# Optimization experiments

Measured on AMD Instinct MI355X. Metric: run time of the kernel, lower is better.

Reference implementation:

```python
import jax, jax.numpy as jnp
import numpy as np

N, M, K = 500000, 8, 16


def setup_inputs() -> dict:
    key = jax.random.key(0)
    kp, kq, ka, kx = jax.random.split(key, 4)
    p = jax.random.normal(kp, (N, M), dtype=jnp.float32)
    q = jax.random.normal(kq, (N, M), dtype=jnp.float32)
    # scale transitions to be contractive so the length-N recurrence is stable
    a = 0.2 * jax.random.normal(ka, (N, M, M), dtype=jnp.float32)
    x = jax.random.normal(kx, (N, K), dtype=jnp.float32)
    return {"p": p, "q": q, "a": a, "x": x}


def reference(p, q, a, x):
    # StrictLowerTriQSM.matmul: y_i = p_i @ f_i, with recurrence
    # f_{i+1} = a_i @ f_i + outer(q_i, x_i), f_0 = 0.  f has shape (M, K).
    def impl(f, data):
        qi, ai, xi = data
        return ai @ f + jnp.outer(qi, xi), f

    init = jnp.zeros((M, x.shape[1]), dtype=x.dtype)
    _, f = jax.lax.scan(impl, init, (q, a, x))  # f: (N, M, K)
    return jnp.einsum("nm,nmk->nk", p, f)
```

## Files before the change

### kernel.cpp

```cpp
#include <hip/hip_runtime.h>


#define NTOT 500000
#define CHUNK 64
#define NCHUNK 8192
#define G 4
#define NGPC 16
#define GRPSZ 64
#define NGRP 128
#define CLAMPI 499996

#define OFF_AGGA  0u
#define OFF_AGGB  524288u
#define OFF_GAGA  1572864u
#define OFF_GAGB  1581056u

#define AS1(p) ((const __attribute__((address_space(1))) void*)(p))
#define AS3(p) ((__attribute__((address_space(3))) void*)(p))
#define GLOAD_LDS16(gp, lp) __builtin_amdgcn_global_load_lds(AS1(gp), AS3(lp), 16, 0, 0)
#define GLOAD_LDS4(gp, lp)  __builtin_amdgcn_global_load_lds(AS1(gp), AS3(lp), 4, 0, 0)
#define WAIT_VM(n) asm volatile("s_waitcnt vmcnt(" #n ")" ::: "memory")

static __device__ __forceinline__ int iminc(int a, int b) { return a < b ? a : b; }

__global__ __launch_bounds__(256, 4) void k1_aggregate(
    const float* __restrict__ q, const float* __restrict__ a,
    const float* __restrict__ x, float* __restrict__ ws)
{
  __shared__ float sm[4 * 2 * 704];
  const int wv   = (int)(threadIdx.x >> 6);
  const int wave = blockIdx.x * 4 + wv;
  const int lane = (int)(threadIdx.x & 63);
  const int sub  = lane >> 5;
  const int ll   = lane & 31;
  const int c    = wave * 2 + sub;
  const bool isB = ll < 16;
  const bool isA = (ll >= 16) && (ll < 24);
  const int bcol = ll & 15;
  const int acol = (ll - 16) & 7;

  float* wbuf = sm + wv * 1408;
  const int c0 = wave * 2, c1 = c0 + 1;

  float v[8];
#pragma unroll
  for (int m = 0; m < 8; ++m) v[m] = 0.f;
  if (isA) v[acol] = 1.f;

  int cnt = NTOT - c * CHUNK;
  cnt = cnt < 0 ? 0 : (cnt > CHUNK ? CHUNK : cnt);

  auto stage = [&](int g, float* lb) {
    const int b0 = iminc(c0 * CHUNK + g * G, CLAMPI);
    const int b1 = iminc(c1 * CHUNK + g * G, CLAMPI);
    GLOAD_LDS16(a + (size_t)b0 * 64u + lane * 4, lb);
    GLOAD_LDS16(a + (size_t)b1 * 64u + lane * 4, lb + 256);
    GLOAD_LDS4(q + (size_t)(lane < 32 ? b0 : b1) * 8u + ll, lb + 512);
    GLOAD_LDS4(x + (size_t)b0 * 16u + lane, lb + 576);
    GLOAD_LDS4(x + (size_t)b1 * 16u + lane, lb + 640);
  };

  stage(0, wbuf);
#pragma unroll 1
  for (int g = 0; g < NGPC; ++g) {
    float* lb = wbuf + (g & 1) * 704;
    if (g + 1 < NGPC) {
      stage(g + 1, wbuf + ((g + 1) & 1) * 704);
      WAIT_VM(5);
    } else {
      WAIT_VM(0);
    }
#pragma unroll 1
    for (int e = 0; e < G; ++e) {
      const int eg = g * G + e;
      if (eg < cnt) {
        const float* ae = lb + sub * 256 + e * 64;
        const float xk  = lb[576 + sub * 64 + e * 16 + bcol];
        const float* qe = lb + 512 + sub * 32 + e * 8;
        float qv[8];
        *(float4*)&qv[0] = *(const float4*)(qe);
        *(float4*)&qv[4] = *(const float4*)(qe + 4);
        float nv[8];
#pragma unroll
        for (int m = 0; m < 8; ++m) {
          float4 r0 = *(const float4*)(ae + m * 8);
          float4 r1 = *(const float4*)(ae + m * 8 + 4);
          float s = isB ? (qv[m] * xk) : 0.f;
          s += r0.x * v[0] + r0.y * v[1] + r0.z * v[2] + r0.w * v[3]
             + r1.x * v[4] + r1.y * v[5] + r1.z * v[6] + r1.w * v[7];
          nv[m] = s;
        }
#pragma unroll
        for (int m = 0; m < 8; ++m) v[m] = nv[m];
      }
    }
  }

  if (isB) {
    float* dst = ws + OFF_AGGB + (size_t)c * 128u + (size_t)bcol * 8u;
#pragma unroll
    for (int m = 0; m < 8; ++m) dst[m] = v[m];
  } else if (isA) {
    float* dst = ws + OFF_AGGA + (size_t)c * 64u + (size_t)acol * 8u;
#pragma unroll
    for (int m = 0; m < 8; ++m) dst[m] = v[m];
  }
}

__global__ __launch_bounds__(64) void k2a_groupscan(float* __restrict__ ws)
{
  __shared__ float sA[GRPSZ * 64];
  const int g    = blockIdx.x;
  const int lane = (int)(threadIdx.x & 63);
  const bool isB = lane < 16;
  const bool isA = (lane >= 16) && (lane < 24);
  const int bcol = lane & 15;
  const int acol = (lane - 16) & 7;

#pragma unroll 1
  for (int t = 0; t < 16; ++t)
    GLOAD_LDS16(ws + OFF_AGGA + (size_t)g * (GRPSZ * 64u) + t * 256 + lane * 4,
                sA + t * 256);

  float v[8];
#pragma unroll
  for (int m = 0; m < 8; ++m) v[m] = 0.f;
  if (isA) v[acol] = 1.f;

  float4 nb0, nb1;
  {
    const float* s = ws + OFF_AGGB + (size_t)(g * GRPSZ) * 128u + (size_t)bcol * 8u;
    nb0 = *(const float4*)s; nb1 = *(const float4*)(s + 4);
  }
  WAIT_VM(0);

#pragma unroll 1
  for (int j = 0; j < GRPSZ; ++j) {
    const int c = g * GRPSZ + j;
    float bB[8] = {nb0.x, nb0.y, nb0.z, nb0.w, nb1.x, nb1.y, nb1.z, nb1.w};
    if (j + 1 < GRPSZ) {
      const float* s = ws + OFF_AGGB + (size_t)(c + 1) * 128u + (size_t)bcol * 8u;
      nb0 = *(const float4*)s; nb1 = *(const float4*)(s + 4);
    }
    if (isB) {
      float* dst = ws + OFF_AGGB + (size_t)c * 128u + (size_t)bcol * 8u;
#pragma unroll
      for (int m = 0; m < 8; ++m) dst[m] = v[m];
    } else if (isA) {
      float* dst = ws + OFF_AGGA + (size_t)c * 64u + (size_t)acol * 8u;
#pragma unroll
      for (int m = 0; m < 8; ++m) dst[m] = v[m];
    }
    const float* Aj = sA + j * 64;
    float nv[8];
#pragma unroll
    for (int m = 0; m < 8; ++m) nv[m] = 0.f;
#pragma unroll
    for (int t = 0; t < 8; ++t) {
      float4 col0 = *(const float4*)(Aj + t * 8);
      float4 col1 = *(const float4*)(Aj + t * 8 + 4);
      nv[0] += col0.x * v[t]; nv[1] += col0.y * v[t];
      nv[2] += col0.z * v[t]; nv[3] += col0.w * v[t];
      nv[4] += col1.x * v[t]; nv[5] += col1.y * v[t];
      nv[6] += col1.z * v[t]; nv[7] += col1.w * v[t];
    }
    if (isB) {
#pragma unroll
      for (int m = 0; m < 8; ++m) nv[m] += bB[m];
    }
#pragma unroll
    for (int m = 0; m < 8; ++m) v[m] = nv[m];
  }

  if (isB) {
    float* dst = ws + OFF_GAGB + (size_t)g * 128u + (size_t)bcol * 8u;
#pragma unroll
    for (int m = 0; m < 8; ++m) dst[m] = v[m];
  } else if (isA) {
    float* dst = ws + OFF_GAGA + (size_t)g * 64u + (size_t)acol * 8u;
#pragma unroll
    for (int m = 0; m < 8; ++m) dst[m] = v[m];
  }
}

__global__ __launch_bounds__(64) void k2b_topscan(float* __restrict__ ws)
{
  __shared__ float sA[NGRP * 64];
  const int lane = (int)(threadIdx.x & 63);
  const bool isB = lane < 16;
  const bool isA = (lane >= 16) && (lane < 24);
  const int bcol = lane & 15;
  const int acol = (lane - 16) & 7;

#pragma unroll 1
  for (int t = 0; t < 32; ++t)
    GLOAD_LDS16(ws + OFF_GAGA + t * 256 + lane * 4, sA + t * 256);

  float v[8];
#pragma unroll
  for (int m = 0; m < 8; ++m) v[m] = 0.f;
  if (isA) v[acol] = 1.f;

  float4 nb0, nb1;
  {
    const float* s = ws + OFF_GAGB + (size_t)bcol * 8u;
    nb0 = *(const float4*)s; nb1 = *(const float4*)(s + 4);
  }
  WAIT_VM(0);

#pragma unroll 1
  for (int j = 0; j < NGRP; ++j) {
    float bB[8] = {nb0.x, nb0.y, nb0.z, nb0.w, nb1.x, nb1.y, nb1.z, nb1.w};
    if (j + 1 < NGRP) {
      const float* s = ws + OFF_GAGB + (size_t)(j + 1) * 128u + (size_t)bcol * 8u;
      nb0 = *(const float4*)s; nb1 = *(const float4*)(s + 4);
    }
    if (isB) {
      float* dst = ws + OFF_GAGB + (size_t)j * 128u + (size_t)bcol * 8u;
#pragma unroll
      for (int m = 0; m < 8; ++m) dst[m] = v[m];
    }
    const float* Aj = sA + j * 64;
    float nv[8];
#pragma unroll
    for (int m = 0; m < 8; ++m) nv[m] = 0.f;
#pragma unroll
    for (int t = 0; t < 8; ++t) {
      float4 col0 = *(const float4*)(Aj + t * 8);
      float4 col1 = *(const float4*)(Aj + t * 8 + 4);
      nv[0] += col0.x * v[t]; nv[1] += col0.y * v[t];
      nv[2] += col0.z * v[t]; nv[3] += col0.w * v[t];
      nv[4] += col1.x * v[t]; nv[5] += col1.y * v[t];
      nv[6] += col1.z * v[t]; nv[7] += col1.w * v[t];
    }
    if (isB) {
#pragma unroll
      for (int m = 0; m < 8; ++m) nv[m] += bB[m];
    }
#pragma unroll
    for (int m = 0; m < 8; ++m) v[m] = nv[m];
  }
}

#define K3_BQ 1040
#define K3_BP 1172
#define K3_BX 1304
#define K3_BUF 1624
__global__ __launch_bounds__(256, 3) void k3_output(
    const float* __restrict__ p, const float* __restrict__ q,
    const float* __restrict__ a, const float* __restrict__ x,
    const float* __restrict__ ws, float* __restrict__ out)
{
  __shared__ float sm3[4 * 2 * K3_BUF];
  const int wv   = (int)(threadIdx.x >> 6);
  const int wave = blockIdx.x * 4 + wv;
  const int lane = (int)(threadIdx.x & 63);
  const int sub  = lane >> 4;
  const int k    = lane & 15;
  const int c    = wave * 4 + sub;
  const int grp  = c >> 6;

  float* wbuf = sm3 + wv * (2 * K3_BUF);
  const int cb = wave * 4;

  auto stage = [&](int g, float* lb) {
    int b[4];
#pragma unroll
    for (int cc = 0; cc < 4; ++cc) b[cc] = iminc((cb + cc) * CHUNK + g * G, CLAMPI);
    GLOAD_LDS16(a + (size_t)b[0] * 64u + lane * 4, lb);
    GLOAD_LDS16(a + (size_t)b[1] * 64u + lane * 4, lb + 260);
    GLOAD_LDS16(a + (size_t)b[2] * 64u + lane * 4, lb + 520);
    GLOAD_LDS16(a + (size_t)b[3] * 64u + lane * 4, lb + 780);
    GLOAD_LDS4(q + (size_t)(lane < 32 ? b[0] : b[1]) * 8u + (lane & 31), lb + K3_BQ);
    GLOAD_LDS4(q + (size_t)(lane < 32 ? b[2] : b[3]) * 8u + (lane & 31), lb + K3_BQ + 68);
    GLOAD_LDS4(p + (size_t)(lane < 32 ? b[0] : b[1]) * 8u + (lane & 31), lb + K3_BP);
    GLOAD_LDS4(p + (size_t)(lane < 32 ? b[2] : b[3]) * 8u + (lane & 31), lb + K3_BP + 68);
    GLOAD_LDS4(x + (size_t)b[0] * 16u + lane, lb + K3_BX);
    GLOAD_LDS4(x + (size_t)b[1] * 16u + lane, lb + K3_BX + 80);
    GLOAD_LDS4(x + (size_t)b[2] * 16u + lane, lb + K3_BX + 160);
    GLOAD_LDS4(x + (size_t)b[3] * 16u + lane, lb + K3_BX + 240);
  };

  stage(0, wbuf);

  const float* __restrict__ pA = ws + OFF_AGGA + (size_t)c * 64u;
  float af[64];
#pragma unroll
  for (int t = 0; t < 64; ++t) af[t] = pA[t];
  const float* __restrict__ gBp = ws + OFF_GAGB + (size_t)grp * 128u + (size_t)k * 8u;
  const float* __restrict__ lBp = ws + OFF_AGGB + (size_t)c * 128u + (size_t)k * 8u;
  float gcol[8];
#pragma unroll
  for (int t = 0; t < 8; ++t) gcol[t] = gBp[t];
  float f[8];
#pragma unroll
  for (int m = 0; m < 8; ++m) {
    float s = lBp[m];
#pragma unroll
    for (int t = 0; t < 8; ++t) s += af[t * 8 + m] * gcol[t];
    f[m] = s;
  }

  int cnt = NTOT - c * CHUNK;
  cnt = cnt < 0 ? 0 : (cnt > CHUNK ? CHUNK : cnt);

#pragma unroll 1
  for (int g = 0; g < NGPC; ++g) {
    float* lb = wbuf + (g & 1) * K3_BUF;
    if (g + 1 < NGPC) {
      stage(g + 1, wbuf + ((g + 1) & 1) * K3_BUF);
      WAIT_VM(12);
    } else {
      WAIT_VM(0);
    }
#pragma unroll 1
    for (int e = 0; e < G; ++e) {
      const int eg = g * G + e;
      if (eg < cnt) {
        const int i = c * CHUNK + eg;
        const float* ae = lb + sub * 260 + e * 64;
        const float* qe = lb + K3_BQ + (sub >> 1) * 68 + (sub & 1) * 32 + e * 8;
        const float* pe = lb + K3_BP + (sub >> 1) * 68 + (sub & 1) * 32 + e * 8;
        const float xk  = lb[K3_BX + sub * 80 + e * 16 + k];
        float qv[8], pv[8];
        *(float4*)&qv[0] = *(const float4*)(qe);
        *(float4*)&qv[4] = *(const float4*)(qe + 4);
        *(float4*)&pv[0] = *(const float4*)(pe);
        *(float4*)&pv[4] = *(const float4*)(pe + 4);

        float y = 0.f;
#pragma unroll
        for (int m = 0; m < 8; ++m) y += pv[m] * f[m];
        out[(size_t)i * 16u + k] = y;

        float nf[8];
#pragma unroll
        for (int m = 0; m < 8; ++m) {
          float4 r0 = *(const float4*)(ae + m * 8);
          float4 r1 = *(const float4*)(ae + m * 8 + 4);
          float s = qv[m] * xk;
          s += r0.x * f[0] + r0.y * f[1] + r0.z * f[2] + r0.w * f[3]
             + r1.x * f[4] + r1.y * f[5] + r1.z * f[6] + r1.w * f[7];
          nf[m] = s;
        }
#pragma unroll
        for (int m = 0; m < 8; ++m) f[m] = nf[m];
      }
    }
  }
}

extern "C" void kernel_launch(void* const* d_in, const int* in_sizes, int n_in,
                              void* d_out, int out_size, void* d_ws, size_t ws_size,
                              hipStream_t stream)
{
  const float* p = (const float*)d_in[0];
  const float* q = (const float*)d_in[1];
  const float* a = (const float*)d_in[2];
  const float* x = (const float*)d_in[3];
  float* out = (float*)d_out;
  float* ws  = (float*)d_ws;

  hipLaunchKernelGGL(k1_aggregate, dim3(NCHUNK / 2 / 4), dim3(256), 0, stream, q, a, x, ws);
  hipLaunchKernelGGL(k2a_groupscan, dim3(NGRP), dim3(64), 0, stream, ws);
  hipLaunchKernelGGL(k2b_topscan, dim3(1), dim3(64), 0, stream, ws);
  hipLaunchKernelGGL(k3_output, dim3(NCHUNK / 4 / 4), dim3(256), 0, stream, p, q, a, x, ws, out);
}
```

Measured before the change: 196.6 us.

## Triple-buffer LDS prefetch and halve chunks per wave in output kernel

Both the aggregate and output kernels move from double to triple buffering of the global-to-LDS staged loads, keeping two groups of loads in flight to hide more memory latency. The output kernel now handles 2 chunks per wave instead of 4, so half the lanes are idle, and it launches twice as many blocks. It also reads the chunk aggregate matrix directly instead of holding 64 floats in registers, which lowers register pressure and allows 4 waves per SIMD. The trade-off is more LDS per block, half-utilised waves in the output kernel, and more waves doing the same sequential work.

```diff
diff --git a/kernel.cpp b/kernel.cpp
--- a/kernel.cpp
+++ b/kernel.cpp
@@ -27,7 +27,7 @@
     const float* __restrict__ q, const float* __restrict__ a,
     const float* __restrict__ x, float* __restrict__ ws)
 {
-  __shared__ float sm[4 * 2 * 704];
+  __shared__ float sm[4 * 3 * 704];
   const int wv   = (int)(threadIdx.x >> 6);
   const int wave = blockIdx.x * 4 + wv;
   const int lane = (int)(threadIdx.x & 63);
@@ -39,8 +39,10 @@
   const int bcol = ll & 15;
   const int acol = (ll - 16) & 7;
 
-  float* wbuf = sm + wv * 1408;
   const int c0 = wave * 2, c1 = c0 + 1;
+  float* b0 = sm + wv * 2112;
+  float* b1 = b0 + 704;
+  float* b2 = b0 + 1408;
 
   float v[8];
 #pragma unroll
@@ -51,21 +53,24 @@
   cnt = cnt < 0 ? 0 : (cnt > CHUNK ? CHUNK : cnt);
 
   auto stage = [&](int g, float* lb) {
-    const int b0 = iminc(c0 * CHUNK + g * G, CLAMPI);
-    const int b1 = iminc(c1 * CHUNK + g * G, CLAMPI);
-    GLOAD_LDS16(a + (size_t)b0 * 64u + lane * 4, lb);
-    GLOAD_LDS16(a + (size_t)b1 * 64u + lane * 4, lb + 256);
-    GLOAD_LDS4(q + (size_t)(lane < 32 ? b0 : b1) * 8u + ll, lb + 512);
-    GLOAD_LDS4(x + (size_t)b0 * 16u + lane, lb + 576);
-    GLOAD_LDS4(x + (size_t)b1 * 16u + lane, lb + 640);
+    const int e0 = iminc(c0 * CHUNK + g * G, CLAMPI);
+    const int e1 = iminc(c1 * CHUNK + g * G, CLAMPI);
+    GLOAD_LDS16(a + (size_t)e0 * 64u + lane * 4, lb);
+    GLOAD_LDS16(a + (size_t)e1 * 64u + lane * 4, lb + 256);
+    GLOAD_LDS4(q + (size_t)(lane < 32 ? e0 : e1) * 8u + ll, lb + 512);
+    GLOAD_LDS4(x + (size_t)e0 * 16u + lane, lb + 576);
+    GLOAD_LDS4(x + (size_t)e1 * 16u + lane, lb + 640);
   };
 
-  stage(0, wbuf);
+  stage(0, b0);
+  stage(1, b1);
 #pragma unroll 1
   for (int g = 0; g < NGPC; ++g) {
-    float* lb = wbuf + (g & 1) * 704;
-    if (g + 1 < NGPC) {
-      stage(g + 1, wbuf + ((g + 1) & 1) * 704);
+    float* lb = b0;
+    if (g + 2 < NGPC) {
+      stage(g + 2, b2);
+      WAIT_VM(10);
+    } else if (g + 1 < NGPC) {
       WAIT_VM(5);
     } else {
       WAIT_VM(0);
@@ -76,6 +81,7 @@
       if (eg < cnt) {
         const float* ae = lb + sub * 256 + e * 64;
         const float xk  = lb[576 + sub * 64 + e * 16 + bcol];
+        const float xke = isB ? xk : 0.f;
         const float* qe = lb + 512 + sub * 32 + e * 8;
         float qv[8];
         *(float4*)&qv[0] = *(const float4*)(qe);
@@ -85,7 +91,7 @@
         for (int m = 0; m < 8; ++m) {
           float4 r0 = *(const float4*)(ae + m * 8);
           float4 r1 = *(const float4*)(ae + m * 8 + 4);
-          float s = isB ? (qv[m] * xk) : 0.f;
+          float s = qv[m] * xke;
           s += r0.x * v[0] + r0.y * v[1] + r0.z * v[2] + r0.w * v[3]
              + r1.x * v[4] + r1.y * v[5] + r1.z * v[6] + r1.w * v[7];
           nv[m] = s;
@@ -94,6 +100,7 @@
         for (int m = 0; m < 8; ++m) v[m] = nv[m];
       }
     }
+    float* t = b0; b0 = b1; b1 = b2; b2 = t;
   }
 
   if (isB) {
@@ -242,51 +249,45 @@
   }
 }
 
-#define K3_BQ 1040
-#define K3_BP 1172
-#define K3_BX 1304
-#define K3_BUF 1624
-__global__ __launch_bounds__(256, 3) void k3_output(
+#define K3_BQ 520
+#define K3_BP 584
+#define K3_BX 648
+#define K3_BUF 784
+__global__ __launch_bounds__(256, 4) void k3_output(
     const float* __restrict__ p, const float* __restrict__ q,
     const float* __restrict__ a, const float* __restrict__ x,
     const float* __restrict__ ws, float* __restrict__ out)
 {
-  __shared__ float sm3[4 * 2 * K3_BUF];
+  __shared__ float sm3[4 * 3 * K3_BUF];
   const int wv   = (int)(threadIdx.x >> 6);
   const int wave = blockIdx.x * 4 + wv;
   const int lane = (int)(threadIdx.x & 63);
-  const int sub  = lane >> 4;
+  const int sub  = (lane >> 4) & 1;
   const int k    = lane & 15;
-  const int c    = wave * 4 + sub;
+  const bool active = lane < 32;
+  const int c    = wave * 2 + sub;
   const int grp  = c >> 6;
 
-  float* wbuf = sm3 + wv * (2 * K3_BUF);
-  const int cb = wave * 4;
+  const int c0 = wave * 2, c1 = c0 + 1;
+  float* b0 = sm3 + wv * (3 * K3_BUF);
+  float* b1 = b0 + K3_BUF;
+  float* b2 = b0 + 2 * K3_BUF;
 
   auto stage = [&](int g, float* lb) {
-    int b[4];
-#pragma unroll
-    for (int cc = 0; cc < 4; ++cc) b[cc] = iminc((cb + cc) * CHUNK + g * G, CLAMPI);
-    GLOAD_LDS16(a + (size_t)b[0] * 64u + lane * 4, lb);
-    GLOAD_LDS16(a + (size_t)b[1] * 64u + lane * 4, lb + 260);
-    GLOAD_LDS16(a + (size_t)b[2] * 64u + lane * 4, lb + 520);
-    GLOAD_LDS16(a + (size_t)b[3] * 64u + lane * 4, lb + 780);
-    GLOAD_LDS4(q + (size_t)(lane < 32 ? b[0] : b[1]) * 8u + (lane & 31), lb + K3_BQ);
-    GLOAD_LDS4(q + (size_t)(lane < 32 ? b[2] : b[3]) * 8u + (lane & 31), lb + K3_BQ + 68);
-    GLOAD_LDS4(p + (size_t)(lane < 32 ? b[0] : b[1]) * 8u + (lane & 31), lb + K3_BP);
-    GLOAD_LDS4(p + (size_t)(lane < 32 ? b[2] : b[3]) * 8u + (lane & 31), lb + K3_BP + 68);
-    GLOAD_LDS4(x + (size_t)b[0] * 16u + lane, lb + K3_BX);
-    GLOAD_LDS4(x + (size_t)b[1] * 16u + lane, lb + K3_BX + 80);
-    GLOAD_LDS4(x + (size_t)b[2] * 16u + lane, lb + K3_BX + 160);
-    GLOAD_LDS4(x + (size_t)b[3] * 16u + lane, lb + K3_BX + 240);
+    const int e0 = iminc(c0 * CHUNK + g * G, CLAMPI);
+    const int e1 = iminc(c1 * CHUNK + g * G, CLAMPI);
+    GLOAD_LDS16(a + (size_t)e0 * 64u + lane * 4, lb);
+    GLOAD_LDS16(a + (size_t)e1 * 64u + lane * 4, lb + 260);
+    GLOAD_LDS4(q + (size_t)(lane < 32 ? e0 : e1) * 8u + (lane & 31), lb + K3_BQ);
+    GLOAD_LDS4(p + (size_t)(lane < 32 ? e0 : e1) * 8u + (lane & 31), lb + K3_BP);
+    GLOAD_LDS4(x + (size_t)e0 * 16u + lane, lb + K3_BX);
+    GLOAD_LDS4(x + (size_t)e1 * 16u + lane, lb + K3_BX + 64);
   };
 
-  stage(0, wbuf);
-
-  const float* __restrict__ pA = ws + OFF_AGGA + (size_t)c * 64u;
-  float af[64];
-#pragma unroll
-  for (int t = 0; t < 64; ++t) af[t] = pA[t];
+  stage(0, b0);
+  stage(1, b1);
+
+  const float* __restrict__ pA  = ws + OFF_AGGA + (size_t)c * 64u;
   const float* __restrict__ gBp = ws + OFF_GAGB + (size_t)grp * 128u + (size_t)k * 8u;
   const float* __restrict__ lBp = ws + OFF_AGGB + (size_t)c * 128u + (size_t)k * 8u;
   float gcol[8];
@@ -294,11 +295,16 @@
   for (int t = 0; t < 8; ++t) gcol[t] = gBp[t];
   float f[8];
 #pragma unroll
-  for (int m = 0; m < 8; ++m) {
-    float s = lBp[m];
-#pragma unroll
-    for (int t = 0; t < 8; ++t) s += af[t * 8 + m] * gcol[t];
-    f[m] = s;
+  for (int m = 0; m < 8; ++m) f[m] = lBp[m];
+#pragma unroll
+  for (int t = 0; t < 8; ++t) {
+    float4 col0 = *(const float4*)(pA + t * 8);
+    float4 col1 = *(const float4*)(pA + t * 8 + 4);
+    const float gt = gcol[t];
+    f[0] += col0.x * gt; f[1] += col0.y * gt;
+    f[2] += col0.z * gt; f[3] += col0.w * gt;
+    f[4] += col1.x * gt; f[5] += col1.y * gt;
+    f[6] += col1.z * gt; f[7] += col1.w * gt;
   }
 
   int cnt = NTOT - c * CHUNK;
@@ -306,10 +312,12 @@
 
 #pragma unroll 1
   for (int g = 0; g < NGPC; ++g) {
-    float* lb = wbuf + (g & 1) * K3_BUF;
-    if (g + 1 < NGPC) {
-      stage(g + 1, wbuf + ((g + 1) & 1) * K3_BUF);
+    float* lb = b0;
+    if (g + 2 < NGPC) {
+      stage(g + 2, b2);
       WAIT_VM(12);
+    } else if (g + 1 < NGPC) {
+      WAIT_VM(6);
     } else {
       WAIT_VM(0);
     }
@@ -319,9 +327,9 @@
       if (eg < cnt) {
         const int i = c * CHUNK + eg;
         const float* ae = lb + sub * 260 + e * 64;
-        const float* qe = lb + K3_BQ + (sub >> 1) * 68 + (sub & 1) * 32 + e * 8;
-        const float* pe = lb + K3_BP + (sub >> 1) * 68 + (sub & 1) * 32 + e * 8;
-        const float xk  = lb[K3_BX + sub * 80 + e * 16 + k];
+        const float* qe = lb + K3_BQ + sub * 32 + e * 8;
+        const float* pe = lb + K3_BP + sub * 32 + e * 8;
+        const float xk  = lb[K3_BX + sub * 64 + e * 16 + k];
         float qv[8], pv[8];
         *(float4*)&qv[0] = *(const float4*)(qe);
         *(float4*)&qv[4] = *(const float4*)(qe + 4);
@@ -331,7 +339,7 @@
         float y = 0.f;
 #pragma unroll
         for (int m = 0; m < 8; ++m) y += pv[m] * f[m];
-        out[(size_t)i * 16u + k] = y;
+        if (active) out[(size_t)i * 16u + k] = y;
 
         float nf[8];
 #pragma unroll
@@ -347,6 +355,7 @@
         for (int m = 0; m < 8; ++m) f[m] = nf[m];
       }
     }
+    float* t = b0; b0 = b1; b1 = b2; b2 = t;
   }
 }
 
@@ -364,5 +373,5 @@
   hipLaunchKernelGGL(k1_aggregate, dim3(NCHUNK / 2 / 4), dim3(256), 0, stream, q, a, x, ws);
   hipLaunchKernelGGL(k2a_groupscan, dim3(NGRP), dim3(64), 0, stream, ws);
   hipLaunchKernelGGL(k2b_topscan, dim3(1), dim3(64), 0, stream, ws);
-  hipLaunchKernelGGL(k3_output, dim3(NCHUNK / 4 / 4), dim3(256), 0, stream, p, q, a, x, ws, out);
-}
+  hipLaunchKernelGGL(k3_output, dim3(NCHUNK / 2 / 4), dim3(256), 0, stream, p, q, a, x, ws, out);
+}
```

Measured after the change: 215.5 us. 1.1x slower.

## Triple-buffer LDS staging and pack four chunks per wave in aggregate kernel

Applied to the files above, without the earlier changes.

Both streaming kernels move from double- to triple-buffered global-to-LDS staging, with two stages in flight, to hide more memory latency. The aggregate kernel now handles four chunks per wave: each lane carries both a B column and an A column in registers, so all 64 lanes do useful work and the grid is halved. The output kernel reads the A aggregate with float4 loads instead of holding 64 registers. In exchange, LDS per block grows, the launch-bounds occupancy hint drops to 2, and per-lane work in k1 doubles.

```diff
diff --git a/kernel.cpp b/kernel.cpp
--- a/kernel.cpp
+++ b/kernel.cpp
@@ -23,87 +23,107 @@
 
 static __device__ __forceinline__ int iminc(int a, int b) { return a < b ? a : b; }
 
-__global__ __launch_bounds__(256, 4) void k1_aggregate(
+#define K1_BQ 1040
+#define K1_BX 1176
+#define K1_BUF 1480
+__global__ __launch_bounds__(256, 2) void k1_aggregate(
     const float* __restrict__ q, const float* __restrict__ a,
     const float* __restrict__ x, float* __restrict__ ws)
 {
-  __shared__ float sm[4 * 2 * 704];
+  __shared__ float sm[4 * 3 * K1_BUF];
   const int wv   = (int)(threadIdx.x >> 6);
   const int wave = blockIdx.x * 4 + wv;
   const int lane = (int)(threadIdx.x & 63);
-  const int sub  = lane >> 5;
-  const int ll   = lane & 31;
-  const int c    = wave * 2 + sub;
-  const bool isB = ll < 16;
-  const bool isA = (ll >= 16) && (ll < 24);
-  const int bcol = ll & 15;
-  const int acol = (ll - 16) & 7;
-
-  float* wbuf = sm + wv * 1408;
-  const int c0 = wave * 2, c1 = c0 + 1;
-
-  float v[8];
-#pragma unroll
-  for (int m = 0; m < 8; ++m) v[m] = 0.f;
-  if (isA) v[acol] = 1.f;
+  const int g    = lane >> 4;
+  const int ll   = lane & 15;
+  const int c    = wave * 4 + g;
+  const bool hasA = ll >= 8;
+  const int acol = ll & 7;
+
+  const int cb = wave * 4;
+  float* b0 = sm + wv * (3 * K1_BUF);
+  float* b1 = b0 + K1_BUF;
+  float* b2 = b0 + 2 * K1_BUF;
+
+  float vB[8], vA[8];
+#pragma unroll
+  for (int m = 0; m < 8; ++m) { vB[m] = 0.f; vA[m] = 0.f; }
+  if (hasA) vA[acol] = 1.f;
 
   int cnt = NTOT - c * CHUNK;
   cnt = cnt < 0 ? 0 : (cnt > CHUNK ? CHUNK : cnt);
 
-  auto stage = [&](int g, float* lb) {
-    const int b0 = iminc(c0 * CHUNK + g * G, CLAMPI);
-    const int b1 = iminc(c1 * CHUNK + g * G, CLAMPI);
-    GLOAD_LDS16(a + (size_t)b0 * 64u + lane * 4, lb);
-    GLOAD_LDS16(a + (size_t)b1 * 64u + lane * 4, lb + 256);
-    GLOAD_LDS4(q + (size_t)(lane < 32 ? b0 : b1) * 8u + ll, lb + 512);
-    GLOAD_LDS4(x + (size_t)b0 * 16u + lane, lb + 576);
-    GLOAD_LDS4(x + (size_t)b1 * 16u + lane, lb + 640);
+  auto stage = [&](int gg, float* lb) {
+    int b[4];
+#pragma unroll
+    for (int cc = 0; cc < 4; ++cc) b[cc] = iminc((cb + cc) * CHUNK + gg * G, CLAMPI);
+    GLOAD_LDS16(a + (size_t)b[0] * 64u + lane * 4, lb);
+    GLOAD_LDS16(a + (size_t)b[1] * 64u + lane * 4, lb + 260);
+    GLOAD_LDS16(a + (size_t)b[2] * 64u + lane * 4, lb + 520);
+    GLOAD_LDS16(a + (size_t)b[3] * 64u + lane * 4, lb + 780);
+    GLOAD_LDS4(q + (size_t)(lane < 32 ? b[0] : b[1]) * 8u + (lane & 31), lb + K1_BQ);
+    GLOAD_LDS4(q + (size_t)(lane < 32 ? b[2] : b[3]) * 8u + (lane & 31), lb + K1_BQ + 68);
+    GLOAD_LDS4(x + (size_t)b[0] * 16u + lane, lb + K1_BX);
+    GLOAD_LDS4(x + (size_t)b[1] * 16u + lane, lb + K1_BX + 80);
+    GLOAD_LDS4(x + (size_t)b[2] * 16u + lane, lb + K1_BX + 160);
+    GLOAD_LDS4(x + (size_t)b[3] * 16u + lane, lb + K1_BX + 240);
   };
 
-  stage(0, wbuf);
-#pragma unroll 1
-  for (int g = 0; g < NGPC; ++g) {
-    float* lb = wbuf + (g & 1) * 704;
-    if (g + 1 < NGPC) {
-      stage(g + 1, wbuf + ((g + 1) & 1) * 704);
-      WAIT_VM(5);
+  stage(0, b0);
+  stage(1, b1);
+#pragma unroll 1
+  for (int gg = 0; gg < NGPC; ++gg) {
+    float* lb = b0;
+    if (gg + 2 < NGPC) {
+      stage(gg + 2, b2);
+      WAIT_VM(20);
+    } else if (gg + 1 < NGPC) {
+      WAIT_VM(10);
     } else {
       WAIT_VM(0);
     }
+    const float* ablk = lb + g * 260;
+    const float* qblk = lb + K1_BQ + (g >> 1) * 68 + (g & 1) * 32;
+    const float* xblk = lb + K1_BX + g * 80;
 #pragma unroll 1
     for (int e = 0; e < G; ++e) {
-      const int eg = g * G + e;
+      const int eg = gg * G + e;
       if (eg < cnt) {
-        const float* ae = lb + sub * 256 + e * 64;
-        const float xk  = lb[576 + sub * 64 + e * 16 + bcol];
-        const float* qe = lb + 512 + sub * 32 + e * 8;
+        const float* ae = ablk + e * 64;
+        const float xk  = xblk[e * 16 + ll];
+        const float* qe = qblk + e * 8;
         float qv[8];
         *(float4*)&qv[0] = *(const float4*)(qe);
         *(float4*)&qv[4] = *(const float4*)(qe + 4);
-        float nv[8];
+        float nB[8], nA[8];
 #pragma unroll
         for (int m = 0; m < 8; ++m) {
           float4 r0 = *(const float4*)(ae + m * 8);
           float4 r1 = *(const float4*)(ae + m * 8 + 4);
-          float s = isB ? (qv[m] * xk) : 0.f;
-          s += r0.x * v[0] + r0.y * v[1] + r0.z * v[2] + r0.w * v[3]
-             + r1.x * v[4] + r1.y * v[5] + r1.z * v[6] + r1.w * v[7];
-          nv[m] = s;
+          float sB = qv[m] * xk;
+          sB += r0.x * vB[0] + r0.y * vB[1] + r0.z * vB[2] + r0.w * vB[3]
+              + r1.x * vB[4] + r1.y * vB[5] + r1.z * vB[6] + r1.w * vB[7];
+          nB[m] = sB;
+          float sA = r0.x * vA[0] + r0.y * vA[1] + r0.z * vA[2] + r0.w * vA[3]
+                   + r1.x * vA[4] + r1.y * vA[5] + r1.z * vA[6] + r1.w * vA[7];
+          nA[m] = sA;
         }
 #pragma unroll
-        for (int m = 0; m < 8; ++m) v[m] = nv[m];
+        for (int m = 0; m < 8; ++m) { vB[m] = nB[m]; vA[m] = nA[m]; }
       }
     }
-  }
-
-  if (isB) {
-    float* dst = ws + OFF_AGGB + (size_t)c * 128u + (size_t)bcol * 8u;
-#pragma unroll
-    for (int m = 0; m < 8; ++m) dst[m] = v[m];
-  } else if (isA) {
+    float* t = b0; b0 = b1; b1 = b2; b2 = t;
+  }
+
+  {
+    float* dst = ws + OFF_AGGB + (size_t)c * 128u + (size_t)ll * 8u;
+#pragma unroll
+    for (int m = 0; m < 8; ++m) dst[m] = vB[m];
+  }
+  if (hasA) {
     float* dst = ws + OFF_AGGA + (size_t)c * 64u + (size_t)acol * 8u;
 #pragma unroll
-    for (int m = 0; m < 8; ++m) dst[m] = v[m];
+    for (int m = 0; m < 8; ++m) dst[m] = vA[m];
   }
 }
 
@@ -243,30 +263,32 @@
 }
 
 #define K3_BQ 1040
-#define K3_BP 1172
-#define K3_BX 1304
-#define K3_BUF 1624
-__global__ __launch_bounds__(256, 3) void k3_output(
+#define K3_BP 1176
+#define K3_BX 1312
+#define K3_BUF 1616
+__global__ __launch_bounds__(256, 2) void k3_output(
     const float* __restrict__ p, const float* __restrict__ q,
     const float* __restrict__ a, const float* __restrict__ x,
     const float* __restrict__ ws, float* __restrict__ out)
 {
-  __shared__ float sm3[4 * 2 * K3_BUF];
+  __shared__ float sm3[4 * 3 * K3_BUF];
   const int wv   = (int)(threadIdx.x >> 6);
   const int wave = blockIdx.x * 4 + wv;
   const int lane = (int)(threadIdx.x & 63);
-  const int sub  = lane >> 4;
+  const int g    = lane >> 4;
   const int k    = lane & 15;
-  const int c    = wave * 4 + sub;
+  const int c    = wave * 4 + g;
   const int grp  = c >> 6;
 
-  float* wbuf = sm3 + wv * (2 * K3_BUF);
   const int cb = wave * 4;
-
-  auto stage = [&](int g, float* lb) {
+  float* b0 = sm3 + wv * (3 * K3_BUF);
+  float* b1 = b0 + K3_BUF;
+  float* b2 = b0 + 2 * K3_BUF;
+
+  auto stage = [&](int gg, float* lb) {
     int b[4];
 #pragma unroll
-    for (int cc = 0; cc < 4; ++cc) b[cc] = iminc((cb + cc) * CHUNK + g * G, CLAMPI);
+    for (int cc = 0; cc < 4; ++cc) b[cc] = iminc((cb + cc) * CHUNK + gg * G, CLAMPI);
     GLOAD_LDS16(a + (size_t)b[0] * 64u + lane * 4, lb);
     GLOAD_LDS16(a + (size_t)b[1] * 64u + lane * 4, lb + 260);
     GLOAD_LDS16(a + (size_t)b[2] * 64u + lane * 4, lb + 520);
@@ -281,12 +303,10 @@
     GLOAD_LDS4(x + (size_t)b[3] * 16u + lane, lb + K3_BX + 240);
   };
 
-  stage(0, wbuf);
-
-  const float* __restrict__ pA = ws + OFF_AGGA + (size_t)c * 64u;
-  float af[64];
-#pragma unroll
-  for (int t = 0; t < 64; ++t) af[t] = pA[t];
+  stage(0, b0);
+  stage(1, b1);
+
+  const float* __restrict__ pA  = ws + OFF_AGGA + (size_t)c * 64u;
   const float* __restrict__ gBp = ws + OFF_GAGB + (size_t)grp * 128u + (size_t)k * 8u;
   const float* __restrict__ lBp = ws + OFF_AGGB + (size_t)c * 128u + (size_t)k * 8u;
   float gcol[8];
@@ -294,34 +314,45 @@
   for (int t = 0; t < 8; ++t) gcol[t] = gBp[t];
   float f[8];
 #pragma unroll
-  for (int m = 0; m < 8; ++m) {
-    float s = lBp[m];
-#pragma unroll
-    for (int t = 0; t < 8; ++t) s += af[t * 8 + m] * gcol[t];
-    f[m] = s;
+  for (int m = 0; m < 8; ++m) f[m] = lBp[m];
+#pragma unroll
+  for (int t = 0; t < 8; ++t) {
+    float4 col0 = *(const float4*)(pA + t * 8);
+    float4 col1 = *(const float4*)(pA + t * 8 + 4);
+    const float gt = gcol[t];
+    f[0] += col0.x * gt; f[1] += col0.y * gt;
+    f[2] += col0.z * gt; f[3] += col0.w * gt;
+    f[4] += col1.x * gt; f[5] += col1.y * gt;
+    f[6] += col1.z * gt; f[7] += col1.w * gt;
   }
 
   int cnt = NTOT - c * CHUNK;
   cnt = cnt < 0 ? 0 : (cnt > CHUNK ? CHUNK : cnt);
 
 #pragma unroll 1
-  for (int g = 0; g < NGPC; ++g) {
-    float* lb = wbuf + (g & 1) * K3_BUF;
-    if (g + 1 < NGPC) {
-      stage(g + 1, wbuf + ((g + 1) & 1) * K3_BUF);
+  for (int gg = 0; gg < NGPC; ++gg) {
+    float* lb = b0;
+    if (gg + 2 < NGPC) {
+      stage(gg + 2, b2);
+      WAIT_VM(24);
+    } else if (gg + 1 < NGPC) {
       WAIT_VM(12);
     } else {
       WAIT_VM(0);
     }
+    const float* ablk = lb + g * 260;
+    const float* qblk = lb + K3_BQ + (g >> 1) * 68 + (g & 1) * 32;
+    const float* pblk = lb + K3_BP + (g >> 1) * 68 + (g & 1) * 32;
+    const float* xblk = lb + K3_BX + g * 80;
 #pragma unroll 1
     for (int e = 0; e < G; ++e) {
-      const int eg = g * G + e;
+      const int eg = gg * G + e;
       if (eg < cnt) {
         const int i = c * CHUNK + eg;
-        const float* ae = lb + sub * 260 + e * 64;
-        const float* qe = lb + K3_BQ + (sub >> 1) * 68 + (sub & 1) * 32 + e * 8;
-        const float* pe = lb + K3_BP + (sub >> 1) * 68 + (sub & 1) * 32 + e * 8;
-        const float xk  = lb[K3_BX + sub * 80 + e * 16 + k];
+        const float* ae = ablk + e * 64;
+        const float* qe = qblk + e * 8;
+        const float* pe = pblk + e * 8;
+        const float xk  = xblk[e * 16 + k];
         float qv[8], pv[8];
         *(float4*)&qv[0] = *(const float4*)(qe);
         *(float4*)&qv[4] = *(const float4*)(qe + 4);
@@ -347,6 +378,7 @@
         for (int m = 0; m < 8; ++m) f[m] = nf[m];
       }
     }
+    float* t = b0; b0 = b1; b1 = b2; b2 = t;
   }
 }
 
@@ -361,7 +393,7 @@
   float* out = (float*)d_out;
   float* ws  = (float*)d_ws;
 
-  hipLaunchKernelGGL(k1_aggregate, dim3(NCHUNK / 2 / 4), dim3(256), 0, stream, q, a, x, ws);
+  hipLaunchKernelGGL(k1_aggregate, dim3(NCHUNK / 4 / 4), dim3(256), 0, stream, q, a, x, ws);
   hipLaunchKernelGGL(k2a_groupscan, dim3(NGRP), dim3(64), 0, stream, ws);
   hipLaunchKernelGGL(k2b_topscan, dim3(1), dim3(64), 0, stream, ws);
   hipLaunchKernelGGL(k3_output, dim3(NCHUNK / 4 / 4), dim3(256), 0, stream, p, q, a, x, ws, out);
```

After: 197.5 us. No clear change (+0.4%).
